# Kernel tuning notes

Hardware: AMD Instinct MI355X
Metric: run time of the kernel (lower is better)

Reference implementation:

```python
import jax, jax.numpy as jnp
import numpy as np

B, H, S, D = 2, 12, 2048, 64


def setup_inputs() -> dict:
    key = jax.random.key(0)
    kq, kk, kv = jax.random.split(key, 3)
    q = jax.random.normal(kq, (B, H, S, D), dtype=jnp.float32)
    k = jax.random.normal(kk, (B, H, S, D), dtype=jnp.float32)
    v = jax.random.normal(kv, (B, H, S, D), dtype=jnp.float32)
    mask = jnp.zeros((1, 1, S, S), dtype=jnp.float32)  # additive mask
    return {"q": q, "k": k, "v": v, "mask": mask}


def reference(q, k, v, mask):
    # scaled dot-product attention, materializing full [B,H,S,S] weights
    dk = jnp.sqrt(jnp.asarray(q.shape[-1], dtype=q.dtype))
    logits = jnp.einsum("bhsd,bhtd->bhst", q, k) / dk
    logits = logits + mask  # additive mask, broadcast over B,H
    we = jax.nn.softmax(logits, axis=-1)
    out = jnp.einsum("bhst,bhtd->bhsd", we, v)
    return (out, we)
```

## Files before the change

kernel.cpp:

```cpp
#include <hip/hip_runtime.h>


typedef short          s16x8 __attribute__((ext_vector_type(8)));
typedef unsigned short u16x8 __attribute__((ext_vector_type(8)));
typedef float          f32x4 __attribute__((ext_vector_type(4)));

#define kS   2048
#define kD   64
#define kBH  24
#define OUT_ELEMS (kBH * kS * kD)

static __device__ __forceinline__ unsigned short f2bf(float f) {
    union { float f; unsigned u; } x; x.f = f;
    return (unsigned short)((x.u + 0x7fffu + ((x.u >> 16) & 1u)) >> 16);
}

static __device__ __forceinline__ u16x8 cvt8(const float4 f0, const float4 f1) {
    u16x8 r;
    r[0] = f2bf(f0.x); r[1] = f2bf(f0.y); r[2] = f2bf(f0.z); r[3] = f2bf(f0.w);
    r[4] = f2bf(f1.x); r[5] = f2bf(f1.y); r[6] = f2bf(f1.z); r[7] = f2bf(f1.w);
    return r;
}

__global__ __launch_bounds__(256)
void attn_fused(const float* __restrict__ Qg, const float* __restrict__ Kg,
                const float* __restrict__ Vg, const float* __restrict__ Mg,
                float* __restrict__ Og, float* __restrict__ Wg)
{
    __shared__ __align__(16) unsigned short k_sh[32 * 64];
    __shared__ __align__(16) unsigned short vt_sh[64 * 32];
    __shared__ __align__(16) unsigned short p_sh[4][16 * 40];

    const int tid  = threadIdx.x;
    const int wv   = tid >> 6;
    const int lane = tid & 63;
    const int g    = lane >> 4;
    const int c    = lane & 15;

    const int wg = ((int)blockIdx.x & 7) * 96 + ((int)blockIdx.x >> 3);
    const int bh = wg >> 5;
    const int qb = wg & 31;
    const int q0 = qb * 64 + wv * 16;

    s16x8 aQ[2];
    {
        const float* qp = Qg + ((size_t)(bh * kS + q0 + c)) * kD + g * 8;
        #pragma unroll
        for (int h = 0; h < 2; ++h) {
            float4 f0 = *(const float4*)(qp + h * 32);
            float4 f1 = *(const float4*)(qp + h * 32 + 4);
            union { u16x8 u; s16x8 s; } t; t.u = cvt8(f0, f1);
            aQ[h] = t.s;
        }
    }

    const int sr = tid >> 3;
    const int sc = (tid & 7) * 8;
    const float* kstage = Kg + ((size_t)bh * kS + sr) * kD + sc;
    const float* vstage = Vg + ((size_t)bh * kS + sr) * kD + sc;
    const unsigned kaddr_w = (unsigned)((sr * 128 + sc * 2) ^ ((sr & 7) << 4));
    const float* mrow = Mg + (size_t)(q0 + g * 4) * kS;

    float sm[4] = {0.f, 0.f, 0.f, 0.f};
    for (int t0 = 0; t0 < kS; t0 += 32) {
        __syncthreads();
        {
            const float* src = kstage + (size_t)t0 * kD;
            *(u16x8*)((char*)k_sh + kaddr_w) = cvt8(*(const float4*)src, *(const float4*)(src + 4));
        }
        __syncthreads();
        #pragma unroll
        for (int tt = 0; tt < 2; ++tt) {
            const int row = tt * 16 + c;
            f32x4 acc = {0.f, 0.f, 0.f, 0.f};
            #pragma unroll
            for (int h = 0; h < 2; ++h) {
                const unsigned a = (unsigned)((row * 128 + h * 64 + g * 16) ^ ((row & 7) << 4));
                s16x8 bK = *(const s16x8*)((const char*)k_sh + a);
                acc = __builtin_amdgcn_mfma_f32_16x16x32_bf16(aQ[h], bK, acc, 0, 0, 0);
            }
            const int t = t0 + tt * 16 + c;
            #pragma unroll
            for (int j = 0; j < 4; ++j)
                sm[j] += __expf(acc[j] * 0.125f + mrow[(size_t)j * kS + t]);
        }
    }
    #pragma unroll
    for (int j = 0; j < 4; ++j) {
        float s = sm[j];
        s += __shfl_xor(s, 1);
        s += __shfl_xor(s, 2);
        s += __shfl_xor(s, 4);
        s += __shfl_xor(s, 8);
        sm[j] = 1.0f / s;
    }

    f32x4 accO[4];
    #pragma unroll
    for (int dt = 0; dt < 4; ++dt) accO[dt] = f32x4{0.f, 0.f, 0.f, 0.f};

    float* wrow = Wg + ((size_t)(bh * kS + q0 + g * 4)) * kS;

    for (int t0 = 0; t0 < kS; t0 += 32) {
        __syncthreads();
        {
            const float* srck = kstage + (size_t)t0 * kD;
            *(u16x8*)((char*)k_sh + kaddr_w) = cvt8(*(const float4*)srck, *(const float4*)(srck + 4));
            const float* srcv = vstage + (size_t)t0 * kD;
            u16x8 vb = cvt8(*(const float4*)srcv, *(const float4*)(srcv + 4));
            #pragma unroll
            for (int i = 0; i < 8; ++i)
                vt_sh[(sc + i) * 32 + sr] = vb[i];
        }
        __syncthreads();

        #pragma unroll
        for (int tt = 0; tt < 2; ++tt) {
            const int row = tt * 16 + c;
            f32x4 acc = {0.f, 0.f, 0.f, 0.f};
            #pragma unroll
            for (int h = 0; h < 2; ++h) {
                const unsigned a = (unsigned)((row * 128 + h * 64 + g * 16) ^ ((row & 7) << 4));
                s16x8 bK = *(const s16x8*)((const char*)k_sh + a);
                acc = __builtin_amdgcn_mfma_f32_16x16x32_bf16(aQ[h], bK, acc, 0, 0, 0);
            }
            const int t = t0 + tt * 16 + c;
            #pragma unroll
            for (int j = 0; j < 4; ++j) {
                const float p = __expf(acc[j] * 0.125f + mrow[(size_t)j * kS + t]) * sm[j];
                __builtin_nontemporal_store(p, wrow + (size_t)j * kS + t);
                p_sh[wv][(g * 4 + j) * 40 + tt * 16 + c] = f2bf(p);
            }
        }

        s16x8 pa = *(const s16x8*)((const char*)&p_sh[wv][0] + c * 80 + g * 16);

        #pragma unroll
        for (int dt = 0; dt < 4; ++dt) {
            s16x8 bV = *(const s16x8*)((const char*)vt_sh + (dt * 16 + c) * 64 + g * 16);
            accO[dt] = __builtin_amdgcn_mfma_f32_16x16x32_bf16(pa, bV, accO[dt], 0, 0, 0);
        }
    }

    float* orow = Og + ((size_t)(bh * kS + q0 + g * 4)) * kD + c;
    #pragma unroll
    for (int dt = 0; dt < 4; ++dt) {
        #pragma unroll
        for (int j = 0; j < 4; ++j)
            __builtin_nontemporal_store(accO[dt][j], orow + (size_t)j * kD + dt * 16);
    }
}

extern "C" void kernel_launch(void* const* d_in, const int* in_sizes, int n_in,
                              void* d_out, int out_size, void* d_ws, size_t ws_size,
                              hipStream_t stream) {
    const float* q = (const float*)d_in[0];
    const float* k = (const float*)d_in[1];
    const float* v = (const float*)d_in[2];
    const float* m = (const float*)d_in[3];
    float* out = (float*)d_out;
    float* we  = out + OUT_ELEMS;
    attn_fused<<<dim3(kBH * 32), dim3(256), 0, stream>>>(q, k, v, m, out, we);
}
```

Measured before the change: 171.5 us.

## Double-buffer K/V LDS tiles and transpose S-tile for vectorized weight stores

```diff
diff --git a/kernel.cpp b/kernel.cpp
--- a/kernel.cpp
+++ b/kernel.cpp
@@ -3,6 +3,7 @@
 
 typedef short          s16x8 __attribute__((ext_vector_type(8)));
 typedef unsigned short u16x8 __attribute__((ext_vector_type(8)));
+typedef unsigned short u16x4 __attribute__((ext_vector_type(4)));
 typedef float          f32x4 __attribute__((ext_vector_type(4)));
 
 #define kS   2048
@@ -27,8 +28,8 @@
                 const float* __restrict__ Vg, const float* __restrict__ Mg,
                 float* __restrict__ Og, float* __restrict__ Wg)
 {
-    __shared__ __align__(16) unsigned short k_sh[32 * 64];
-    __shared__ __align__(16) unsigned short vt_sh[64 * 32];
+    __shared__ __align__(16) unsigned short k_sh[2][32 * 64];
+    __shared__ __align__(16) unsigned short vt_sh[2][64 * 32];
     __shared__ __align__(16) unsigned short p_sh[4][16 * 40];
 
     const int tid  = threadIdx.x;
@@ -59,16 +60,23 @@
     const float* kstage = Kg + ((size_t)bh * kS + sr) * kD + sc;
     const float* vstage = Vg + ((size_t)bh * kS + sr) * kD + sc;
     const unsigned kaddr_w = (unsigned)((sr * 128 + sc * 2) ^ ((sr & 7) << 4));
-    const float* mrow = Mg + (size_t)(q0 + g * 4) * kS;
-
-    float sm[4] = {0.f, 0.f, 0.f, 0.f};
+    const float* mrow = Mg + (size_t)(q0 + c) * kS;
+
+    {
+        const float* src = kstage;
+        *(u16x8*)((char*)k_sh[0] + kaddr_w) = cvt8(*(const float4*)src, *(const float4*)(src + 4));
+    }
+    __syncthreads();
+
+    float sm = 0.f;
+    int cur = 0;
     for (int t0 = 0; t0 < kS; t0 += 32) {
-        __syncthreads();
-        {
-            const float* src = kstage + (size_t)t0 * kD;
-            *(u16x8*)((char*)k_sh + kaddr_w) = cvt8(*(const float4*)src, *(const float4*)(src + 4));
-        }
-        __syncthreads();
+        const bool nxt = (t0 + 32) < kS;
+        float4 kf0, kf1;
+        if (nxt) {
+            const float* src = kstage + (size_t)(t0 + 32) * kD;
+            kf0 = *(const float4*)src; kf1 = *(const float4*)(src + 4);
+        }
         #pragma unroll
         for (int tt = 0; tt < 2; ++tt) {
             const int row = tt * 16 + c;
@@ -76,43 +84,56 @@
             #pragma unroll
             for (int h = 0; h < 2; ++h) {
                 const unsigned a = (unsigned)((row * 128 + h * 64 + g * 16) ^ ((row & 7) << 4));
-                s16x8 bK = *(const s16x8*)((const char*)k_sh + a);
-                acc = __builtin_amdgcn_mfma_f32_16x16x32_bf16(aQ[h], bK, acc, 0, 0, 0);
+                s16x8 bK = *(const s16x8*)((const char*)k_sh[cur] + a);
+                acc = __builtin_amdgcn_mfma_f32_16x16x32_bf16(bK, aQ[h], acc, 0, 0, 0);
             }
-            const int t = t0 + tt * 16 + c;
-            #pragma unroll
-            for (int j = 0; j < 4; ++j)
-                sm[j] += __expf(acc[j] * 0.125f + mrow[(size_t)j * kS + t]);
-        }
-    }
-    #pragma unroll
-    for (int j = 0; j < 4; ++j) {
-        float s = sm[j];
-        s += __shfl_xor(s, 1);
-        s += __shfl_xor(s, 2);
-        s += __shfl_xor(s, 4);
-        s += __shfl_xor(s, 8);
-        sm[j] = 1.0f / s;
-    }
+            const float4 mk = *(const float4*)(mrow + t0 + tt * 16 + g * 4);
+            sm += __expf(acc[0] * 0.125f + mk.x);
+            sm += __expf(acc[1] * 0.125f + mk.y);
+            sm += __expf(acc[2] * 0.125f + mk.z);
+            sm += __expf(acc[3] * 0.125f + mk.w);
+        }
+        if (nxt) {
+            *(u16x8*)((char*)k_sh[cur ^ 1] + kaddr_w) = cvt8(kf0, kf1);
+            __syncthreads();
+            cur ^= 1;
+        }
+    }
+    sm += __shfl_xor(sm, 16);
+    sm += __shfl_xor(sm, 32);
+    const float sminv = 1.0f / sm;
 
     f32x4 accO[4];
     #pragma unroll
     for (int dt = 0; dt < 4; ++dt) accO[dt] = f32x4{0.f, 0.f, 0.f, 0.f};
 
-    float* wrow = Wg + ((size_t)(bh * kS + q0 + g * 4)) * kS;
-
+    float* wrow = Wg + ((size_t)(bh * kS + q0 + c)) * kS;
+
+    __syncthreads();
+    {
+        const float* srck = kstage;
+        *(u16x8*)((char*)k_sh[0] + kaddr_w) = cvt8(*(const float4*)srck, *(const float4*)(srck + 4));
+        const float* srcv = vstage;
+        u16x8 vb = cvt8(*(const float4*)srcv, *(const float4*)(srcv + 4));
+        #pragma unroll
+        for (int i = 0; i < 8; ++i) {
+            const int d = sc + i;
+            const unsigned b = (unsigned)((d * 64 + sr * 2) ^ (((d >> 3) & 7) << 4));
+            *(unsigned short*)((char*)vt_sh[0] + b) = vb[i];
+        }
+    }
+    __syncthreads();
+
+    cur = 0;
     for (int t0 = 0; t0 < kS; t0 += 32) {
-        __syncthreads();
-        {
-            const float* srck = kstage + (size_t)t0 * kD;
-            *(u16x8*)((char*)k_sh + kaddr_w) = cvt8(*(const float4*)srck, *(const float4*)(srck + 4));
-            const float* srcv = vstage + (size_t)t0 * kD;
-            u16x8 vb = cvt8(*(const float4*)srcv, *(const float4*)(srcv + 4));
-            #pragma unroll
-            for (int i = 0; i < 8; ++i)
-                vt_sh[(sc + i) * 32 + sr] = vb[i];
-        }
-        __syncthreads();
+        const bool nxt = (t0 + 32) < kS;
+        float4 kf0, kf1, vf0, vf1;
+        if (nxt) {
+            const float* srck = kstage + (size_t)(t0 + 32) * kD;
+            kf0 = *(const float4*)srck; kf1 = *(const float4*)(srck + 4);
+            const float* srcv = vstage + (size_t)(t0 + 32) * kD;
+            vf0 = *(const float4*)srcv; vf1 = *(const float4*)(srcv + 4);
+        }
 
         #pragma unroll
         for (int tt = 0; tt < 2; ++tt) {
@@ -121,24 +142,41 @@
             #pragma unroll
             for (int h = 0; h < 2; ++h) {
                 const unsigned a = (unsigned)((row * 128 + h * 64 + g * 16) ^ ((row & 7) << 4));
-                s16x8 bK = *(const s16x8*)((const char*)k_sh + a);
-                acc = __builtin_amdgcn_mfma_f32_16x16x32_bf16(aQ[h], bK, acc, 0, 0, 0);
+                s16x8 bK = *(const s16x8*)((const char*)k_sh[cur] + a);
+                acc = __builtin_amdgcn_mfma_f32_16x16x32_bf16(bK, aQ[h], acc, 0, 0, 0);
             }
-            const int t = t0 + tt * 16 + c;
+            const float4 mk = *(const float4*)(mrow + t0 + tt * 16 + g * 4);
+            f32x4 p;
+            p[0] = __expf(acc[0] * 0.125f + mk.x) * sminv;
+            p[1] = __expf(acc[1] * 0.125f + mk.y) * sminv;
+            p[2] = __expf(acc[2] * 0.125f + mk.z) * sminv;
+            p[3] = __expf(acc[3] * 0.125f + mk.w) * sminv;
+            __builtin_nontemporal_store(p, (f32x4*)(wrow + t0 + tt * 16 + g * 4));
+            u16x4 pb;
+            pb[0] = f2bf(p[0]); pb[1] = f2bf(p[1]); pb[2] = f2bf(p[2]); pb[3] = f2bf(p[3]);
+            *(u16x4*)&p_sh[wv][c * 40 + tt * 16 + g * 4] = pb;
+        }
+
+        s16x8 pa = *(const s16x8*)((const char*)&p_sh[wv][0] + c * 80 + g * 16);
+        #pragma unroll
+        for (int dt = 0; dt < 4; ++dt) {
+            const int d = dt * 16 + c;
+            const unsigned b = (unsigned)((d * 64 + g * 16) ^ (((d >> 3) & 7) << 4));
+            s16x8 bV = *(const s16x8*)((const char*)vt_sh[cur] + b);
+            accO[dt] = __builtin_amdgcn_mfma_f32_16x16x32_bf16(pa, bV, accO[dt], 0, 0, 0);
+        }
+
+        if (nxt) {
+            *(u16x8*)((char*)k_sh[cur ^ 1] + kaddr_w) = cvt8(kf0, kf1);
+            u16x8 vb = cvt8(vf0, vf1);
             #pragma unroll
-            for (int j = 0; j < 4; ++j) {
-                const float p = __expf(acc[j] * 0.125f + mrow[(size_t)j * kS + t]) * sm[j];
-                __builtin_nontemporal_store(p, wrow + (size_t)j * kS + t);
-                p_sh[wv][(g * 4 + j) * 40 + tt * 16 + c] = f2bf(p);
+            for (int i = 0; i < 8; ++i) {
+                const int d = sc + i;
+                const unsigned b = (unsigned)((d * 64 + sr * 2) ^ (((d >> 3) & 7) << 4));
+                *(unsigned short*)((char*)vt_sh[cur ^ 1] + b) = vb[i];
             }
-        }
-
-        s16x8 pa = *(const s16x8*)((const char*)&p_sh[wv][0] + c * 80 + g * 16);
-
-        #pragma unroll
-        for (int dt = 0; dt < 4; ++dt) {
-            s16x8 bV = *(const s16x8*)((const char*)vt_sh + (dt * 16 + c) * 64 + g * 16);
-            accO[dt] = __builtin_amdgcn_mfma_f32_16x16x32_bf16(pa, bV, accO[dt], 0, 0, 0);
+            __syncthreads();
+            cur ^= 1;
         }
     }
 
```

Measured after the change: 188.0 us. 9.6% more time.

## Split key dimension across two wave groups per block with cross-group reduction

Applied to the files above, without the earlier changes.

```diff
diff --git a/kernel.cpp b/kernel.cpp
--- a/kernel.cpp
+++ b/kernel.cpp
@@ -8,7 +8,14 @@
 #define kS   2048
 #define kD   64
 #define kBH  24
+#define kTH  1024
 #define OUT_ELEMS (kBH * kS * kD)
+
+#define K_OFF   0
+#define VT_OFF  16384
+#define P_OFF   32768
+#define SM_OFF  43008
+#define POOL_SZ 43520
 
 static __device__ __forceinline__ unsigned short f2bf(float f) {
     union { float f; unsigned u; } x; x.f = f;
@@ -22,17 +29,17 @@
     return r;
 }
 
-__global__ __launch_bounds__(256)
+__global__ __launch_bounds__(512)
 void attn_fused(const float* __restrict__ Qg, const float* __restrict__ Kg,
                 const float* __restrict__ Vg, const float* __restrict__ Mg,
                 float* __restrict__ Og, float* __restrict__ Wg)
 {
-    __shared__ __align__(16) unsigned short k_sh[32 * 64];
-    __shared__ __align__(16) unsigned short vt_sh[64 * 32];
-    __shared__ __align__(16) unsigned short p_sh[4][16 * 40];
+    __shared__ __align__(16) unsigned char pool[POOL_SZ];
 
     const int tid  = threadIdx.x;
     const int wv   = tid >> 6;
+    const int qsub = wv & 3;
+    const int th   = wv >> 2;
     const int lane = tid & 63;
     const int g    = lane >> 4;
     const int c    = lane & 15;
@@ -40,7 +47,13 @@
     const int wg = ((int)blockIdx.x & 7) * 96 + ((int)blockIdx.x >> 3);
     const int bh = wg >> 5;
     const int qb = wg & 31;
-    const int q0 = qb * 64 + wv * 16;
+    const int q0 = qb * 64 + qsub * 16;
+    const int tb = th * kTH;
+
+    unsigned short* k_sh  = (unsigned short*)(pool + K_OFF)  + th * (32 * 64);
+    unsigned short* vt_sh = (unsigned short*)(pool + VT_OFF) + th * (64 * 32);
+    unsigned short* p_shw = (unsigned short*)(pool + P_OFF)  + wv * (16 * 40);
+    float*          sm_sh = (float*)(pool + SM_OFF);
 
     s16x8 aQ[2];
     {
@@ -54,15 +67,16 @@
         }
     }
 
-    const int sr = tid >> 3;
-    const int sc = (tid & 7) * 8;
-    const float* kstage = Kg + ((size_t)bh * kS + sr) * kD + sc;
-    const float* vstage = Vg + ((size_t)bh * kS + sr) * kD + sc;
+    const int tg = tid & 255;
+    const int sr = tg >> 3;
+    const int sc = (tg & 7) * 8;
+    const float* kstage = Kg + ((size_t)(bh * kS + tb + sr)) * kD + sc;
+    const float* vstage = Vg + ((size_t)(bh * kS + tb + sr)) * kD + sc;
     const unsigned kaddr_w = (unsigned)((sr * 128 + sc * 2) ^ ((sr & 7) << 4));
-    const float* mrow = Mg + (size_t)(q0 + g * 4) * kS;
+    const float* mrow = Mg + (size_t)(q0 + g * 4) * kS + tb;
 
     float sm[4] = {0.f, 0.f, 0.f, 0.f};
-    for (int t0 = 0; t0 < kS; t0 += 32) {
+    for (int t0 = 0; t0 < kTH; t0 += 32) {
         __syncthreads();
         {
             const float* src = kstage + (size_t)t0 * kD;
@@ -92,16 +106,26 @@
         s += __shfl_xor(s, 2);
         s += __shfl_xor(s, 4);
         s += __shfl_xor(s, 8);
-        sm[j] = 1.0f / s;
-    }
+        sm[j] = s;
+    }
+    if (c == 0) {
+        #pragma unroll
+        for (int j = 0; j < 4; ++j)
+            sm_sh[wv * 16 + g * 4 + j] = sm[j];
+    }
+    __syncthreads();
+    float sminv[4];
+    #pragma unroll
+    for (int j = 0; j < 4; ++j)
+        sminv[j] = 1.0f / (sm_sh[qsub * 16 + g * 4 + j] + sm_sh[64 + qsub * 16 + g * 4 + j]);
 
     f32x4 accO[4];
     #pragma unroll
     for (int dt = 0; dt < 4; ++dt) accO[dt] = f32x4{0.f, 0.f, 0.f, 0.f};
 
-    float* wrow = Wg + ((size_t)(bh * kS + q0 + g * 4)) * kS;
-
-    for (int t0 = 0; t0 < kS; t0 += 32) {
+    float* wrow = Wg + ((size_t)(bh * kS + q0 + g * 4)) * kS + tb;
+
+    for (int t0 = 0; t0 < kTH; t0 += 32) {
         __syncthreads();
         {
             const float* srck = kstage + (size_t)t0 * kD;
@@ -109,8 +133,11 @@
             const float* srcv = vstage + (size_t)t0 * kD;
             u16x8 vb = cvt8(*(const float4*)srcv, *(const float4*)(srcv + 4));
             #pragma unroll
-            for (int i = 0; i < 8; ++i)
-                vt_sh[(sc + i) * 32 + sr] = vb[i];
+            for (int i = 0; i < 8; ++i) {
+                const int d = sc + i;
+                const unsigned b = (unsigned)((d * 64 + sr * 2) ^ (((d >> 3) & 7) << 4));
+                *(unsigned short*)((char*)vt_sh + b) = vb[i];
+            }
         }
         __syncthreads();
 
@@ -127,27 +154,41 @@
             const int t = t0 + tt * 16 + c;
             #pragma unroll
             for (int j = 0; j < 4; ++j) {
-                const float p = __expf(acc[j] * 0.125f + mrow[(size_t)j * kS + t]) * sm[j];
+                const float p = __expf(acc[j] * 0.125f + mrow[(size_t)j * kS + t]) * sminv[j];
                 __builtin_nontemporal_store(p, wrow + (size_t)j * kS + t);
-                p_sh[wv][(g * 4 + j) * 40 + tt * 16 + c] = f2bf(p);
-            }
-        }
-
-        s16x8 pa = *(const s16x8*)((const char*)&p_sh[wv][0] + c * 80 + g * 16);
-
+                p_shw[(g * 4 + j) * 40 + tt * 16 + c] = f2bf(p);
+            }
+        }
+
+        s16x8 pa = *(const s16x8*)((const char*)p_shw + c * 80 + g * 16);
         #pragma unroll
         for (int dt = 0; dt < 4; ++dt) {
-            s16x8 bV = *(const s16x8*)((const char*)vt_sh + (dt * 16 + c) * 64 + g * 16);
+            const int d = dt * 16 + c;
+            const unsigned b = (unsigned)((d * 64 + g * 16) ^ (((d >> 3) & 7) << 4));
+            s16x8 bV = *(const s16x8*)((const char*)vt_sh + b);
             accO[dt] = __builtin_amdgcn_mfma_f32_16x16x32_bf16(pa, bV, accO[dt], 0, 0, 0);
         }
     }
 
-    float* orow = Og + ((size_t)(bh * kS + q0 + g * 4)) * kD + c;
-    #pragma unroll
-    for (int dt = 0; dt < 4; ++dt) {
-        #pragma unroll
-        for (int j = 0; j < 4; ++j)
-            __builtin_nontemporal_store(accO[dt][j], orow + (size_t)j * kD + dt * 16);
+    __syncthreads();
+    float* oacc = (float*)pool;
+    if (th == 1) {
+        #pragma unroll
+        for (int dt = 0; dt < 4; ++dt)
+            #pragma unroll
+            for (int j = 0; j < 4; ++j)
+                oacc[(qsub * 64 + lane) * 20 + dt * 4 + j] = accO[dt][j];
+    }
+    __syncthreads();
+    if (th == 0) {
+        float* orow = Og + ((size_t)(bh * kS + q0 + g * 4)) * kD + c;
+        #pragma unroll
+        for (int dt = 0; dt < 4; ++dt)
+            #pragma unroll
+            for (int j = 0; j < 4; ++j) {
+                const float v = accO[dt][j] + oacc[(qsub * 64 + lane) * 20 + dt * 4 + j];
+                __builtin_nontemporal_store(v, orow + (size_t)j * kD + dt * 16);
+            }
     }
 }
 
@@ -160,5 +201,5 @@
     const float* m = (const float*)d_in[3];
     float* out = (float*)d_out;
     float* we  = out + OUT_ELEMS;
-    attn_fused<<<dim3(kBH * 32), dim3(256), 0, stream>>>(q, k, v, m, out, we);
-}
+    attn_fused<<<dim3(kBH * 32), dim3(512), 0, stream>>>(q, k, v, m, out, we);
+}
```

After: 198.3 us. 1.16x slower.

## Split key dimension across waves and read K/V directly from global memory

Applied to the files above, without the earlier changes.

```diff
diff --git a/kernel.cpp b/kernel.cpp
--- a/kernel.cpp
+++ b/kernel.cpp
@@ -1,4 +1,5 @@
 #include <hip/hip_runtime.h>
+#include <hip/hip_bf16.h>
 
 
 typedef short          s16x8 __attribute__((ext_vector_type(8)));
@@ -8,27 +9,30 @@
 #define kS   2048
 #define kD   64
 #define kBH  24
+#define kTQ  512
 #define OUT_ELEMS (kBH * kS * kD)
 
 static __device__ __forceinline__ unsigned short f2bf(float f) {
-    union { float f; unsigned u; } x; x.f = f;
-    return (unsigned short)((x.u + 0x7fffu + ((x.u >> 16) & 1u)) >> 16);
+    __hip_bfloat16 h = __float2bfloat16(f);
+    return *reinterpret_cast<unsigned short*>(&h);
 }
 
-static __device__ __forceinline__ u16x8 cvt8(const float4 f0, const float4 f1) {
-    u16x8 r;
-    r[0] = f2bf(f0.x); r[1] = f2bf(f0.y); r[2] = f2bf(f0.z); r[3] = f2bf(f0.w);
-    r[4] = f2bf(f1.x); r[5] = f2bf(f1.y); r[6] = f2bf(f1.z); r[7] = f2bf(f1.w);
-    return r;
+static __device__ __forceinline__ s16x8 ld8bf(const float* p) {
+    float4 a = *(const float4*)p;
+    float4 b = *(const float4*)(p + 4);
+    union { u16x8 u; s16x8 s; } t;
+    t.u[0] = f2bf(a.x); t.u[1] = f2bf(a.y); t.u[2] = f2bf(a.z); t.u[3] = f2bf(a.w);
+    t.u[4] = f2bf(b.x); t.u[5] = f2bf(b.y); t.u[6] = f2bf(b.z); t.u[7] = f2bf(b.w);
+    return t.s;
 }
 
-__global__ __launch_bounds__(256)
+__global__ __launch_bounds__(256, 6)
 void attn_fused(const float* __restrict__ Qg, const float* __restrict__ Kg,
                 const float* __restrict__ Vg, const float* __restrict__ Mg,
                 float* __restrict__ Og, float* __restrict__ Wg)
 {
-    __shared__ __align__(16) unsigned short k_sh[32 * 64];
-    __shared__ __align__(16) unsigned short vt_sh[64 * 32];
+    __shared__ float sm_sh[4][16];
+    __shared__ __align__(16) float oacc[3][64 * 16];
     __shared__ __align__(16) unsigned short p_sh[4][16 * 40];
 
     const int tid  = threadIdx.x;
@@ -37,48 +41,28 @@
     const int g    = lane >> 4;
     const int c    = lane & 15;
 
-    const int wg = ((int)blockIdx.x & 7) * 96 + ((int)blockIdx.x >> 3);
-    const int bh = wg >> 5;
-    const int qb = wg & 31;
-    const int q0 = qb * 64 + wv * 16;
+    const int wg = ((int)blockIdx.x & 7) * 384 + ((int)blockIdx.x >> 3);
+    const int bh = wg >> 7;
+    const int q0 = (wg & 127) * 16;
+    const int tq = wv * kTQ;
 
+    const float* qp = Qg + ((size_t)(bh * kS + q0 + c)) * kD + g * 8;
     s16x8 aQ[2];
-    {
-        const float* qp = Qg + ((size_t)(bh * kS + q0 + c)) * kD + g * 8;
-        #pragma unroll
-        for (int h = 0; h < 2; ++h) {
-            float4 f0 = *(const float4*)(qp + h * 32);
-            float4 f1 = *(const float4*)(qp + h * 32 + 4);
-            union { u16x8 u; s16x8 s; } t; t.u = cvt8(f0, f1);
-            aQ[h] = t.s;
-        }
-    }
+    aQ[0] = ld8bf(qp);
+    aQ[1] = ld8bf(qp + 32);
 
-    const int sr = tid >> 3;
-    const int sc = (tid & 7) * 8;
-    const float* kstage = Kg + ((size_t)bh * kS + sr) * kD + sc;
-    const float* vstage = Vg + ((size_t)bh * kS + sr) * kD + sc;
-    const unsigned kaddr_w = (unsigned)((sr * 128 + sc * 2) ^ ((sr & 7) << 4));
+    const float* Kbh  = Kg + (size_t)bh * kS * kD;
+    const float* Vbh  = Vg + (size_t)bh * kS * kD;
     const float* mrow = Mg + (size_t)(q0 + g * 4) * kS;
 
     float sm[4] = {0.f, 0.f, 0.f, 0.f};
-    for (int t0 = 0; t0 < kS; t0 += 32) {
-        __syncthreads();
-        {
-            const float* src = kstage + (size_t)t0 * kD;
-            *(u16x8*)((char*)k_sh + kaddr_w) = cvt8(*(const float4*)src, *(const float4*)(src + 4));
-        }
-        __syncthreads();
+    for (int t0 = tq; t0 < tq + kTQ; t0 += 32) {
         #pragma unroll
         for (int tt = 0; tt < 2; ++tt) {
-            const int row = tt * 16 + c;
+            const float* kp = Kbh + (size_t)(t0 + tt * 16 + c) * kD + g * 8;
             f32x4 acc = {0.f, 0.f, 0.f, 0.f};
-            #pragma unroll
-            for (int h = 0; h < 2; ++h) {
-                const unsigned a = (unsigned)((row * 128 + h * 64 + g * 16) ^ ((row & 7) << 4));
-                s16x8 bK = *(const s16x8*)((const char*)k_sh + a);
-                acc = __builtin_amdgcn_mfma_f32_16x16x32_bf16(aQ[h], bK, acc, 0, 0, 0);
-            }
+            acc = __builtin_amdgcn_mfma_f32_16x16x32_bf16(aQ[0], ld8bf(kp),      acc, 0, 0, 0);
+            acc = __builtin_amdgcn_mfma_f32_16x16x32_bf16(aQ[1], ld8bf(kp + 32), acc, 0, 0, 0);
             const int t = t0 + tt * 16 + c;
             #pragma unroll
             for (int j = 0; j < 4; ++j)
@@ -92,62 +76,77 @@
         s += __shfl_xor(s, 2);
         s += __shfl_xor(s, 4);
         s += __shfl_xor(s, 8);
-        sm[j] = 1.0f / s;
+        sm[j] = s;
     }
+    if (c == 0) {
+        #pragma unroll
+        for (int j = 0; j < 4; ++j) sm_sh[wv][g * 4 + j] = sm[j];
+    }
+    __syncthreads();
+    float sminv[4];
+    #pragma unroll
+    for (int j = 0; j < 4; ++j)
+        sminv[j] = 1.0f / (sm_sh[0][g * 4 + j] + sm_sh[1][g * 4 + j] +
+                           sm_sh[2][g * 4 + j] + sm_sh[3][g * 4 + j]);
 
     f32x4 accO[4];
     #pragma unroll
     for (int dt = 0; dt < 4; ++dt) accO[dt] = f32x4{0.f, 0.f, 0.f, 0.f};
 
     float* wrow = Wg + ((size_t)(bh * kS + q0 + g * 4)) * kS;
+    unsigned short* p_shw = p_sh[wv];
 
-    for (int t0 = 0; t0 < kS; t0 += 32) {
-        __syncthreads();
-        {
-            const float* srck = kstage + (size_t)t0 * kD;
-            *(u16x8*)((char*)k_sh + kaddr_w) = cvt8(*(const float4*)srck, *(const float4*)(srck + 4));
-            const float* srcv = vstage + (size_t)t0 * kD;
-            u16x8 vb = cvt8(*(const float4*)srcv, *(const float4*)(srcv + 4));
-            #pragma unroll
-            for (int i = 0; i < 8; ++i)
-                vt_sh[(sc + i) * 32 + sr] = vb[i];
-        }
-        __syncthreads();
-
+    for (int t0 = tq; t0 < tq + kTQ; t0 += 32) {
         #pragma unroll
         for (int tt = 0; tt < 2; ++tt) {
-            const int row = tt * 16 + c;
+            const float* kp = Kbh + (size_t)(t0 + tt * 16 + c) * kD + g * 8;
             f32x4 acc = {0.f, 0.f, 0.f, 0.f};
-            #pragma unroll
-            for (int h = 0; h < 2; ++h) {
-                const unsigned a = (unsigned)((row * 128 + h * 64 + g * 16) ^ ((row & 7) << 4));
-                s16x8 bK = *(const s16x8*)((const char*)k_sh + a);
-                acc = __builtin_amdgcn_mfma_f32_16x16x32_bf16(aQ[h], bK, acc, 0, 0, 0);
-            }
+            acc = __builtin_amdgcn_mfma_f32_16x16x32_bf16(aQ[0], ld8bf(kp),      acc, 0, 0, 0);
+            acc = __builtin_amdgcn_mfma_f32_16x16x32_bf16(aQ[1], ld8bf(kp + 32), acc, 0, 0, 0);
             const int t = t0 + tt * 16 + c;
             #pragma unroll
             for (int j = 0; j < 4; ++j) {
-                const float p = __expf(acc[j] * 0.125f + mrow[(size_t)j * kS + t]) * sm[j];
+                const float p = __expf(acc[j] * 0.125f + mrow[(size_t)j * kS + t]) * sminv[j];
                 __builtin_nontemporal_store(p, wrow + (size_t)j * kS + t);
-                p_sh[wv][(g * 4 + j) * 40 + tt * 16 + c] = f2bf(p);
+                p_shw[(g * 4 + j) * 40 + tt * 16 + c] = f2bf(p);
             }
         }
 
-        s16x8 pa = *(const s16x8*)((const char*)&p_sh[wv][0] + c * 80 + g * 16);
+        s16x8 pa = *(const s16x8*)((const char*)p_shw + c * 80 + g * 16);
 
+        const float* vb = Vbh + (size_t)(t0 + g * 8) * kD + c;
         #pragma unroll
         for (int dt = 0; dt < 4; ++dt) {
-            s16x8 bV = *(const s16x8*)((const char*)vt_sh + (dt * 16 + c) * 64 + g * 16);
-            accO[dt] = __builtin_amdgcn_mfma_f32_16x16x32_bf16(pa, bV, accO[dt], 0, 0, 0);
+            union { u16x8 u; s16x8 s; } bv;
+            #pragma unroll
+            for (int j = 0; j < 8; ++j)
+                bv.u[j] = f2bf(vb[(size_t)j * kD + dt * 16]);
+            accO[dt] = __builtin_amdgcn_mfma_f32_16x16x32_bf16(pa, bv.s, accO[dt], 0, 0, 0);
         }
     }
 
-    float* orow = Og + ((size_t)(bh * kS + q0 + g * 4)) * kD + c;
-    #pragma unroll
-    for (int dt = 0; dt < 4; ++dt) {
+    if (wv != 0) {
+        float* dst = &oacc[wv - 1][lane * 16];
         #pragma unroll
-        for (int j = 0; j < 4; ++j)
-            __builtin_nontemporal_store(accO[dt][j], orow + (size_t)j * kD + dt * 16);
+        for (int dt = 0; dt < 4; ++dt)
+            #pragma unroll
+            for (int j = 0; j < 4; ++j) dst[dt * 4 + j] = accO[dt][j];
+    }
+    __syncthreads();
+    if (wv == 0) {
+        #pragma unroll
+        for (int w = 0; w < 3; ++w)
+            #pragma unroll
+            for (int dt = 0; dt < 4; ++dt)
+                #pragma unroll
+                for (int j = 0; j < 4; ++j)
+                    accO[dt][j] += oacc[w][lane * 16 + dt * 4 + j];
+        float* orow = Og + ((size_t)(bh * kS + q0 + g * 4)) * kD + c;
+        #pragma unroll
+        for (int dt = 0; dt < 4; ++dt)
+            #pragma unroll
+            for (int j = 0; j < 4; ++j)
+                __builtin_nontemporal_store(accO[dt][j], orow + (size_t)j * kD + dt * 16);
     }
 }
 
@@ -160,5 +159,5 @@
     const float* m = (const float*)d_in[3];
     float* out = (float*)d_out;
     float* we  = out + OUT_ELEMS;
-    attn_fused<<<dim3(kBH * 32), dim3(256), 0, stream>>>(q, k, v, m, out, we);
+    attn_fused<<<dim3(kBH * 128), dim3(256), 0, stream>>>(q, k, v, m, out, we);
 }
```

Result: slower. 449.2 us (+161.9%).
